# Kernel tuning notes

Hardware: AMD Instinct MI355X
Metric: run time of the kernel (lower is better)

The kernel has to match this reference:

```python
import jax, jax.numpy as jnp
from jax import lax
import numpy as np

DN = ('NCHW', 'OIHW', 'NCHW')

def _bn(x, g, b):
    # BatchNorm2d in training mode: batch statistics, biased variance, eps=1e-5
    m = jnp.mean(x, axis=(0, 2, 3), keepdims=True)
    v = jnp.var(x, axis=(0, 2, 3), keepdims=True)
    return g[None, :, None, None] * (x - m) * lax.rsqrt(v + 1e-5) + b[None, :, None, None]

def _conv(x, w, b, s, p):
    y = lax.conv_general_dilated(x, w, (s, s), [(p, p), (p, p)], dimension_numbers=DN)
    return y + b[None, :, None, None]

def _convt(x, w, b, s, p):
    # torch ConvTranspose2d weight layout [in, out, k, k]; equivalent to
    # input-dilated conv with flipped, transposed kernel and padding k-1-p.
    k = w.shape[2]
    pp = k - 1 - p
    w2 = jnp.flip(w, (2, 3)).transpose(1, 0, 2, 3)  # [out, in, k, k]
    y = lax.conv_general_dilated(x, w2, (1, 1), [(pp, pp), (pp, pp)],
                                 lhs_dilation=(s, s), dimension_numbers=DN)
    return y + b[None, :, None, None]

def setup_inputs() -> dict:
    key = jax.random.key(0)
    ks = jax.random.split(key, 16)
    f32 = jnp.float32
    def rn(i, shape, s):
        return jax.random.normal(ks[i], shape, f32) * s
    K = 256
    inp = {
        'x': jax.random.normal(ks[0], (128, 3, 64, 64), f32),
        'codebook': jax.random.uniform(ks[1], (256, 256), f32, -1.0 / K, 1.0 / K),
        'e_w1': rn(2, (64, 3, 3, 3), 0.19), 'e_b1': jnp.zeros((64,), f32),
        'e_g1': jnp.ones((64,), f32), 'e_be1': jnp.zeros((64,), f32),
        'e_w2': rn(3, (128, 64, 4, 4), 0.031), 'e_b2': jnp.zeros((128,), f32),
        'e_g2': jnp.ones((128,), f32), 'e_be2': jnp.zeros((128,), f32),
        'e_w3': rn(4, (192, 128, 4, 4), 0.022), 'e_b3': jnp.zeros((192,), f32),
        'e_g3': jnp.ones((192,), f32), 'e_be3': jnp.zeros((192,), f32),
        'e_w4': rn(5, (256, 192, 1, 1), 0.072), 'e_b4': jnp.zeros((256,), f32),
        'd_w1': rn(6, (256, 192, 1, 1), 0.062), 'd_b1': jnp.zeros((192,), f32),
        'd_g1': jnp.ones((192,), f32), 'd_be1': jnp.zeros((192,), f32),
        'd_w2': rn(7, (192, 128, 4, 4), 0.018), 'd_b2': jnp.zeros((128,), f32),
        'd_g2': jnp.ones((128,), f32), 'd_be2': jnp.zeros((128,), f32),
        'd_w3': rn(8, (128, 64, 4, 4), 0.022), 'd_b3': jnp.zeros((64,), f32),
        'd_g3': jnp.ones((64,), f32), 'd_be3': jnp.zeros((64,), f32),
        'd_w4': rn(9, (3, 64, 3, 3), 0.042), 'd_b4': jnp.zeros((3,), f32),
    }
    return inp

def reference(x, codebook,
              e_w1, e_b1, e_g1, e_be1, e_w2, e_b2, e_g2, e_be2,
              e_w3, e_b3, e_g3, e_be3, e_w4, e_b4,
              d_w1, d_b1, d_g1, d_be1, d_w2, d_b2, d_g2, d_be2,
              d_w3, d_b3, d_g3, d_be3, d_w4, d_b4):
    # encoder
    h = jax.nn.relu(_bn(_conv(x, e_w1, e_b1, 1, 1), e_g1, e_be1))
    h = jax.nn.relu(_bn(_conv(h, e_w2, e_b2, 2, 1), e_g2, e_be2))
    h = jax.nn.relu(_bn(_conv(h, e_w3, e_b3, 2, 1), e_g3, e_be3))
    h = _conv(h, e_w4, e_b4, 1, 0)  # [B, 256, 16, 16]
    B, C, H, W = h.shape
    Z = h.transpose(0, 2, 3, 1).reshape(-1, C)  # [N, D]
    # fused cdist via ||a||^2 + ||b||^2 - 2ab (argmin invariant to const offsets)
    d2 = (jnp.sum(Z * Z, axis=1, keepdims=True)
          + jnp.sum(codebook * codebook, axis=1)[None, :]
          - 2.0 * (Z @ codebook.T))  # [N, K]
    j = jnp.argmin(d2, axis=1)
    Wj = codebook[j]  # [N, D]
    loss_commit = jnp.mean(jnp.sum((Z - lax.stop_gradient(Wj)) ** 2, axis=1))
    loss_code = jnp.mean(jnp.sum((lax.stop_gradient(Z) - Wj) ** 2, axis=1))
    hq = Wj.reshape(B, H, W, C).transpose(0, 3, 1, 2)
    # decoder
    g = jax.nn.relu(_bn(_convt(hq, d_w1, d_b1, 1, 0), d_g1, d_be1))
    g = jax.nn.relu(_bn(_convt(g, d_w2, d_b2, 2, 1), d_g2, d_be2))
    g = jax.nn.relu(_bn(_convt(g, d_w3, d_b3, 2, 1), d_g3, d_be3))
    g = _conv(g, d_w4, d_b4, 1, 1)  # [B, 3, 64, 64]
    return g, loss_commit, loss_code
```

## Files before the change

### kernel.cpp

```cpp
#include <hip/hip_runtime.h>

#define TPB 256

typedef __attribute__((ext_vector_type(4))) float v4f;
typedef __attribute__((ext_vector_type(8))) short v8s;

__device__ __forceinline__ float us2f(unsigned int u) {
    union { unsigned int i; float f; } w; w.i = u << 16; return w.f;
}
__device__ __forceinline__ unsigned short f2us(float f) {
    union { float ff; unsigned int i; } w; w.ff = f;
    unsigned int u = w.i;
    return (unsigned short)((u + 0x7fffu + ((u >> 16) & 1u)) >> 16);
}
__device__ __forceinline__ void gl_lds16(const unsigned short* g, unsigned short* l) {
    __builtin_amdgcn_global_load_lds(
        (const __attribute__((address_space(1))) unsigned int*)g,
        (__attribute__((address_space(3))) unsigned int*)l, 16, 0, 0);
}

template<int CIN, int COUT, int KK>
__global__ __launch_bounds__(TPB) void repack_w(
    const float* __restrict__ w, unsigned short* __restrict__ o)
{
    int idx = blockIdx.x * TPB + threadIdx.x;
    if (idx >= KK * COUT * CIN) return;
    int ci = idx % CIN;
    int co = (idx / CIN) % COUT;
    int kk = idx / (CIN * COUT);
    o[idx] = f2us(w[((size_t)co * CIN + ci) * KK + kk]);
}
template<int CIN, int COUT>
__global__ __launch_bounds__(TPB) void repack_wt1(
    const float* __restrict__ w, unsigned short* __restrict__ o)
{
    int idx = blockIdx.x * TPB + threadIdx.x;
    if (idx >= CIN * COUT) return;
    int ci = idx % CIN;
    int co = idx / CIN;
    o[idx] = f2us(w[(size_t)ci * COUT + co]);
}
template<int CIN, int COUT, int NCB>
__global__ __launch_bounds__(TPB) void repack_wct2(
    const float* __restrict__ w, unsigned short* __restrict__ o)
{
    constexpr int NCI = CIN / 64;
    int idx = blockIdx.x * TPB + threadIdx.x;
    if (idx >= 16 * COUT * CIN) return;
    int e = idx & 7;
    int lane = (idx >> 3) & 63;
    int seg8 = (idx >> 9) & 7;
    int u = idx >> 12;
    int cb = u % NCB;
    int u2 = u / NCB;
    int cc = u2 % NCI;
    int tk = u2 / NCI;
    int kidx = tk & 3, cls = tk >> 2;
    int lr = lane & 15, lc = lane >> 4;
    int kc = seg8 >> 2, sg = seg8 & 3;
    int co = cb * 64 + sg * 16 + lr;
    int ci = cc * 64 + kc * 32 + lc * 8 + e;
    int ohp = cls >> 1, owp = cls & 1;
    int kh = ((ohp + 1) & 1) + 2 * (kidx >> 1);
    int kw = ((owp + 1) & 1) + 2 * (kidx & 1);
    o[idx] = f2us(w[((size_t)ci * COUT + co) * 16 + kh * 4 + kw]);
}

__global__ __launch_bounds__(TPB) void conv_e1(
    const float* __restrict__ x, const float* __restrict__ w,
    const float* __restrict__ bias, unsigned short* __restrict__ y, int N)
{
    __shared__ float wl[27][64];
    int t = threadIdx.x;
    for (int i = t; i < 27 * 64; i += TPB) {
        int co = i & 63;
        int tap = i >> 6;
        int ci = tap / 9, kk = tap % 9;
        wl[tap][co] = w[((size_t)co * 3 + ci) * 9 + kk];
    }
    __syncthreads();
    int p = blockIdx.x * TPB + t;
    int n = p >> 12, oh = (p >> 6) & 63, ow = p & 63;
    float acc[64];
#pragma unroll
    for (int co = 0; co < 64; co++) acc[co] = bias[co];
    for (int ci = 0; ci < 3; ci++) {
#pragma unroll
        for (int kh = 0; kh < 3; kh++) {
            int ih = oh - 1 + kh;
            if ((unsigned)ih >= 64u) continue;
#pragma unroll
            for (int kw = 0; kw < 3; kw++) {
                int iw = ow - 1 + kw;
                if ((unsigned)iw >= 64u) continue;
                float xv = x[(((size_t)n * 3 + ci) * 64 + ih) * 64 + iw];
                int tap = ci * 9 + kh * 3 + kw;
#pragma unroll
                for (int co = 0; co < 64; co++) acc[co] += xv * wl[tap][co];
            }
        }
    }
    unsigned int* yp = (unsigned int*)(y + (size_t)p * 64);
#pragma unroll
    for (int co = 0; co < 64; co += 2)
        yp[co >> 1] = (unsigned int)f2us(acc[co]) | ((unsigned int)f2us(acc[co + 1]) << 16);
}

template<int CIN, int COUT, int HIN, int WIN, int K, int S, int P, int BN,
         int OUTM, int NYB>
__global__ __launch_bounds__(TPB) void conv_mfma(
    const unsigned short* __restrict__ xin, const unsigned short* __restrict__ wrep,
    const float* __restrict__ bias, void* __restrict__ yout, void* __restrict__ yout2,
    float* __restrict__ part, const unsigned short* __restrict__ zpage, int N)
{
    constexpr int HOUT = (HIN + 2 * P - K) / S + 1;
    constexpr int WOUT = (WIN + 2 * P - K) / S + 1;
    constexpr int RN = BN / 32;
    constexpr int BSEG = BN / 16;
    constexpr int NCI = CIN / 64;
    constexpr int NIT = K * K * NCI;
    __shared__ __align__(16) unsigned short Ab[2][16 * 512];
    __shared__ __align__(16) unsigned short Bb[2][2 * BSEG * 512];

    const int t = threadIdx.x, lane = t & 63, wave = t >> 6;
    const int wm = wave >> 1, wn = wave & 1;
    int m0, co0;
    if (NYB == 2) {
        int g = (int)blockIdx.x >> 3, xs = (int)blockIdx.x & 7;
        co0 = (g & 1) * BN;
        m0 = (((g >> 1) << 3) + xs) * 128;
    } else {
        m0 = (int)blockIdx.x * 128;
        co0 = 0;
    }
    const int lr = lane & 15, lc = lane >> 4;

    int n_[2], oh_[2], ow_[2];
#pragma unroll
    for (int i = 0; i < 2; i++) {
        int r = m0 + (wave + 4 * i) * 16 + lr;
        n_[i] = r / (HOUT * WOUT);
        int rem = r % (HOUT * WOUT);
        oh_[i] = rem / WOUT;
        ow_[i] = rem % WOUT;
    }

    v4f acc[4][RN];
#pragma unroll
    for (int i = 0; i < 4; i++)
#pragma unroll
        for (int j = 0; j < RN; j++)
#pragma unroll
            for (int r = 0; r < 4; r++) acc[i][j][r] = 0.f;

    auto do_stage = [&](int it, int pb) {
        const int kk = it / NCI;
        const int ci0 = (it % NCI) * 64;
        const int kh = kk / K, kw = kk % K;
#pragma unroll
        for (int i = 0; i < 2; i++) {
            int ih = oh_[i] * S - P + kh;
            int iw = ow_[i] * S - P + kw;
            bool av = (unsigned)ih < (unsigned)HIN && (unsigned)iw < (unsigned)WIN;
            const unsigned short* b0 = av
                ? xin + (((size_t)n_[i] * HIN + ih) * WIN + iw) * CIN + lc * 8 + ci0
                : zpage;
            gl_lds16(b0, &Ab[pb][(wave + 4 * i) * 512]);
            gl_lds16(av ? b0 + 32 : zpage, &Ab[pb][(8 + wave + 4 * i) * 512]);
        }
        const unsigned short* wt = wrep + (size_t)kk * COUT * CIN;
#pragma unroll
        for (int i = 0; i < 2; i++) {
            int sgb = wave + 4 * i;
            if (sgb < BSEG) {
                const unsigned short* wb =
                    wt + (size_t)(co0 + sgb * 16 + lr) * CIN + ci0 + lc * 8;
                gl_lds16(wb, &Bb[pb][sgb * 512]);
                gl_lds16(wb + 32, &Bb[pb][(BSEG + sgb) * 512]);
            }
        }
    };

    do_stage(0, 0);
    __syncthreads();

    for (int it = 0; it < NIT; ++it) {
        const int pb = it & 1;
        if (it + 1 < NIT) do_stage(it + 1, pb ^ 1);

#pragma unroll
        for (int kc = 0; kc < 2; kc++) {
            v8s a[4], b[RN];
#pragma unroll
            for (int i = 0; i < 4; i++)
                a[i] = *(const v8s*)&Ab[pb][(kc * 8 + wm * 4 + i) * 512 + lane * 8];
#pragma unroll
            for (int j = 0; j < RN; j++)
                b[j] = *(const v8s*)&Bb[pb][(kc * BSEG + wn * RN + j) * 512 + lane * 8];
#pragma unroll
            for (int i = 0; i < 4; i++)
#pragma unroll
                for (int j = 0; j < RN; j++)
                    acc[i][j] = __builtin_amdgcn_mfma_f32_16x16x32_bf16(a[i], b[j], acc[i][j], 0, 0, 0);
        }
        __syncthreads();
    }

    float sloc[RN], qloc[RN];
#pragma unroll
    for (int j = 0; j < RN; j++) { sloc[j] = 0.f; qloc[j] = 0.f; }

#pragma unroll
    for (int i = 0; i < 4; i++) {
        int mr = wm * 64 + i * 16 + (lane >> 4) * 4;
#pragma unroll
        for (int j = 0; j < RN; j++) {
            int col = co0 + wn * (BN / 2) + j * 16 + (lane & 15);
            float bs = bias[col];
#pragma unroll
            for (int r = 0; r < 4; r++) {
                size_t g = (size_t)(m0 + mr + r) * COUT + col;
                float v = acc[i][j][r] + bs;
                if (OUTM == 2) {
                    unsigned short h = f2us(v);
                    ((unsigned short*)yout)[g] = h;
                    ((unsigned short*)yout2)[g] = f2us(v - us2f(h));
                } else {
                    ((unsigned short*)yout)[g] = f2us(v);
                    sloc[j] += v;
                    qloc[j] += v * v;
                }
            }
        }
    }

    if (OUTM == 0) {
        __syncthreads();
        float* red = (float*)Ab;
        for (int i = t; i < 2 * BN; i += TPB) red[i] = 0.f;
        __syncthreads();
#pragma unroll
        for (int j = 0; j < RN; j++) {
            float s = sloc[j], qv = qloc[j];
            s += __shfl_xor(s, 16); s += __shfl_xor(s, 32);
            qv += __shfl_xor(qv, 16); qv += __shfl_xor(qv, 32);
            if ((lane >> 4) == 0) {
                int cl = wn * (BN / 2) + j * 16 + (lane & 15);
                atomicAdd(&red[cl], s);
                atomicAdd(&red[BN + cl], qv);
            }
        }
        __syncthreads();
        int pb = (NYB == 2) ? (m0 >> 7) : (int)blockIdx.x;
        int PB = (NYB == 2) ? ((int)gridDim.x >> 1) : (int)gridDim.x;
        for (int i = t; i < BN; i += TPB) {
            int col = co0 + i;
            part[(size_t)col * PB + pb] = red[i];
            part[(size_t)(COUT + col) * PB + pb] = red[BN + i];
        }
    }
}

template<int CIN, int COUT, int HIN, int WIN, int NCB, int IN_CLS>
__global__ __launch_bounds__(TPB) void convt_c(
    const unsigned short* __restrict__ xin, const unsigned short* __restrict__ wrep,
    const float* __restrict__ bias, unsigned short* __restrict__ yout,
    float* __restrict__ part, const unsigned short* __restrict__ zpage, int N)
{
    constexpr int NCI = CIN / 64;
    constexpr int NIT = 4 * NCI;
    __shared__ __align__(16) unsigned short Ab[2][16 * 1024];
    __shared__ __align__(16) unsigned short Bb[2][8 * 512];

    const int t = threadIdx.x, lane = t & 63, wave = t >> 6;
    int gdec = (int)blockIdx.x >> 3, xs = (int)blockIdx.x & 7;
    int cb = 0;
    if (NCB == 2) { cb = gdec & 1; gdec >>= 1; }
    const int cls = gdec & 3;
    const int tile = ((gdec >> 2) << 3) + xs;
    const int m0 = tile * 256;
    const int co0 = cb * 64;
    const int ohp = cls >> 1, owp = cls & 1;
    const int khb = (ohp + 1) & 1, kwb = (owp + 1) & 1;
    const int dh0 = (ohp + 1 - khb) >> 1, dw0 = (owp + 1 - kwb) >> 1;
    const int lr = lane & 15, lc = lane >> 4;

    const int jr7 = lane >> 3;
    const int sw = ((lane & 7) ^ jr7) * 8;

    int n_[4], i_[4], j0_[4];
#pragma unroll
    for (int q = 0; q < 4; q++) {
        int r0 = m0 + (wave * 4 + q) * 16;
        n_[q] = r0 / (HIN * WIN);
        int rem = r0 % (HIN * WIN);
        i_[q] = rem / WIN;
        j0_[q] = rem % WIN;
    }

    v4f acc[4][4];
#pragma unroll
    for (int i = 0; i < 4; i++)
#pragma unroll
        for (int j = 0; j < 4; j++)
#pragma unroll
            for (int r = 0; r < 4; r++) acc[i][j][r] = 0.f;

    auto stage = [&](int it, int buf) {
        const int tap = it / NCI, cc = it % NCI;
        const int dh = dh0 - (tap >> 1);
        const int dw = dw0 - (tap & 1);
#pragma unroll
        for (int q = 0; q < 4; q++) {
            const int ih = i_[q] + dh;
            const bool ihv = (unsigned)ih < (unsigned)HIN;
#pragma unroll
            for (int h = 0; h < 2; h++) {
                int iw = j0_[q] + h * 8 + jr7 + dw;
                bool av = ihv && (unsigned)iw < (unsigned)WIN;
                size_t ab;
                if (IN_CLS) {
                    int clsi = ((ih & 1) << 1) | (iw & 1);
                    ab = ((((size_t)clsi * N + n_[q]) * (HIN / 2) + (ih >> 1)) * (WIN / 2)
                         + (iw >> 1)) * CIN;
                } else {
                    ab = (((size_t)n_[q] * HIN + ih) * WIN + iw) * CIN;
                }
                const unsigned short* src = av ? xin + ab + cc * 64 + sw : zpage;
                gl_lds16(src, &Ab[buf][(wave * 4 + q) * 1024 + h * 512]);
            }
        }
        const unsigned short* wb = wrep
            + ((size_t)((cls * 4 + tap) * NCI + cc) * NCB + cb) * 4096;
        gl_lds16(wb + wave * 512 + lane * 8, &Bb[buf][wave * 512]);
        gl_lds16(wb + (4 + wave) * 512 + lane * 8, &Bb[buf][(4 + wave) * 512]);
    };

    auto compute = [&](int it, int buf) {
#pragma unroll
        for (int kc = 0; kc < 2; kc++) {
            v8s a[4], b[4];
#pragma unroll
            for (int i = 0; i < 4; i++)
                a[i] = *(const v8s*)&Ab[buf][(wave * 4 + i) * 1024 + lr * 64
                        + ((kc * 32 + lc * 8) ^ ((lr & 7) << 3))];
#pragma unroll
            for (int j = 0; j < 4; j++)
                b[j] = *(const v8s*)&Bb[buf][(kc * 4 + j) * 512 + lane * 8];
#pragma unroll
            for (int i = 0; i < 4; i++)
#pragma unroll
                for (int j = 0; j < 4; j++)
                    acc[i][j] = __builtin_amdgcn_mfma_f32_16x16x32_bf16(a[i], b[j], acc[i][j], 0, 0, 0);
        }
    };

    stage(0, 0);
    __syncthreads();

#pragma unroll
    for (int it = 0; it < NIT; ++it) {
        const int buf = it & 1;
        if (it + 1 < NIT) stage(it + 1, buf ^ 1);
        compute(it, buf);
        __syncthreads();
    }

    float sloc[4], qloc[4];
#pragma unroll
    for (int j = 0; j < 4; j++) { sloc[j] = 0.f; qloc[j] = 0.f; }

    const size_t clsbase = (size_t)cls * N * HIN * WIN;
#pragma unroll
    for (int i = 0; i < 4; i++) {
        int mr = wave * 64 + i * 16 + (lane >> 4) * 4;
#pragma unroll
        for (int j = 0; j < 4; j++) {
            int col = co0 + j * 16 + (lane & 15);
            float bs = bias[col];
#pragma unroll
            for (int r = 0; r < 4; r++) {
                size_t gi = (clsbase + m0 + mr + r) * COUT + col;
                float v = acc[i][j][r] + bs;
                yout[gi] = f2us(v);
                sloc[j] += v;
                qloc[j] += v * v;
            }
        }
    }

    float* red = (float*)Ab;
    for (int i = t; i < 128; i += TPB) red[i] = 0.f;
    __syncthreads();
#pragma unroll
    for (int j = 0; j < 4; j++) {
        float s = sloc[j], qv = qloc[j];
        s += __shfl_xor(s, 16); s += __shfl_xor(s, 32);
        qv += __shfl_xor(qv, 16); qv += __shfl_xor(qv, 32);
        if ((lane >> 4) == 0) {
            int cl = j * 16 + (lane & 15);
            atomicAdd(&red[cl], s);
            atomicAdd(&red[64 + cl], qv);
        }
    }
    __syncthreads();
    const int TILES = (N * HIN * WIN) >> 8;
    const int PB = 4 * TILES;
    const int pb = cls * TILES + tile;
    for (int i = t; i < 64; i += TPB) {
        part[(size_t)(co0 + i) * PB + pb] = red[i];
        part[(size_t)(COUT + co0 + i) * PB + pb] = red[64 + i];
    }
}

template<int C>
__global__ __launch_bounds__(TPB) void bn_stats_p(
    const unsigned short* __restrict__ x, float* __restrict__ part, int M)
{
    constexpr int GPT = C / 8;
    constexpr int RPB = TPB / GPT;
    constexpr int ACT = RPB * GPT;
    __shared__ float sred[2 * C];
    int t = threadIdx.x;
    for (int i = t; i < 2 * C; i += TPB) sred[i] = 0.f;
    __syncthreads();
    if (t < ACT) {
        int g = t % GPT, rs = t / GPT;
        float s[8], sq[8];
#pragma unroll
        for (int k = 0; k < 8; k++) { s[k] = 0.f; sq[k] = 0.f; }
        for (int row = blockIdx.x * RPB + rs; row < M; row += gridDim.x * RPB) {
            int4 v = *(const int4*)(x + (size_t)row * C + g * 8);
            const unsigned int* vu = (const unsigned int*)&v;
#pragma unroll
            for (int k = 0; k < 4; k++) {
                float f0 = us2f(vu[k] & 0xffffu);
                float f1 = us2f(vu[k] >> 16);
                s[2 * k] += f0; sq[2 * k] += f0 * f0;
                s[2 * k + 1] += f1; sq[2 * k + 1] += f1 * f1;
            }
        }
        int c0 = g * 8;
#pragma unroll
        for (int k = 0; k < 8; k++) {
            atomicAdd(&sred[c0 + k], s[k]);
            atomicAdd(&sred[C + c0 + k], sq[k]);
        }
    }
    __syncthreads();
    int B = gridDim.x;
    for (int i = t; i < 2 * C; i += TPB)
        part[(size_t)i * B + blockIdx.x] = sred[i];
}

template<int C>
__global__ __launch_bounds__(64) void bn_reduce2(
    const float* __restrict__ part, float* __restrict__ st, int B)
{
    int i = blockIdx.x;
    int lane = threadIdx.x;
    float s = 0.f;
    for (int b = lane; b < B; b += 64) s += part[(size_t)i * B + b];
#pragma unroll
    for (int off = 1; off < 64; off <<= 1) s += __shfl_xor(s, off);
    if (lane == 0) st[i] = s;
}

template<int C>
__global__ __launch_bounds__(TPB) void bn_apply_v(
    unsigned short* __restrict__ x, const float* __restrict__ st,
    const float* __restrict__ g, const float* __restrict__ be, int M)
{
    __shared__ float sc[C], sh[C];
    int t = threadIdx.x;
    float cnt = (float)M;
    for (int c = t; c < C; c += TPB) {
        float m = st[c] / cnt;
        float v = st[C + c] / cnt - m * m;
        float s = g[c] * rsqrtf(v + 1e-5f);
        sc[c] = s;
        sh[c] = be[c] - m * s;
    }
    __syncthreads();
    constexpr int GPT = C / 8;
    size_t tot = (size_t)M * GPT;
    for (size_t slot = (size_t)blockIdx.x * TPB + t; slot < tot;
         slot += (size_t)gridDim.x * TPB) {
        int c0 = (int)(slot % GPT) * 8;
        int4 v = *(int4*)(x + slot * 8);
        unsigned int* vu = (unsigned int*)&v;
#pragma unroll
        for (int k = 0; k < 4; k++) {
            float f0 = fmaxf(us2f(vu[k] & 0xffffu) * sc[c0 + 2 * k] + sh[c0 + 2 * k], 0.f);
            float f1 = fmaxf(us2f(vu[k] >> 16) * sc[c0 + 2 * k + 1] + sh[c0 + 2 * k + 1], 0.f);
            vu[k] = (unsigned int)f2us(f0) | ((unsigned int)f2us(f1) << 16);
        }
        *(int4*)(x + slot * 8) = v;
    }
}

__global__ __launch_bounds__(TPB) void cb_prep(
    const float* __restrict__ cb, unsigned short* __restrict__ chb,
    unsigned short* __restrict__ clb, float* __restrict__ cn2)
{
    int j = blockIdx.x, d = threadIdx.x;
    float v = cb[j * 256 + d];
    unsigned short h = f2us(v);
    chb[j * 256 + d] = h;
    clb[j * 256 + d] = f2us(v - us2f(h));
    float s = v * v;
#pragma unroll
    for (int off = 1; off < 64; off <<= 1) s += __shfl_xor(s, off);
    __shared__ float p[4];
    if ((d & 63) == 0) p[d >> 6] = s;
    __syncthreads();
    if (d == 0) cn2[j] = p[0] + p[1] + p[2] + p[3];
}

__global__ __launch_bounds__(TPB) void vq_gemm(
    const unsigned short* __restrict__ zh, const unsigned short* __restrict__ zl,
    const unsigned short* __restrict__ chb, const unsigned short* __restrict__ clb,
    const float* __restrict__ cn2, float* __restrict__ valp, int* __restrict__ idxp)
{
    __shared__ __align__(16) unsigned short Ah[2][8 * 512];
    __shared__ __align__(16) unsigned short Al[2][8 * 512];
    __shared__ __align__(16) unsigned short Bh[2][8 * 512];
    __shared__ __align__(16) unsigned short Bl[2][8 * 512];

    const int t = threadIdx.x, lane = t & 63, wave = t >> 6;
    const int wm = wave >> 1, wn = wave & 1;
    const int gdec = (int)blockIdx.x >> 3, xs = (int)blockIdx.x & 7;
    const int cbk = gdec & 1;
    const int m0 = (((gdec >> 1) << 3) + xs) * 128;
    const int co0 = cbk * 128;
    const int lr = lane & 15, lc = lane >> 4;

    size_t a0 = (size_t)(m0 + wave * 16 + lr) * 256 + lc * 8;
    size_t a1 = a0 + 64 * 256;
    size_t b0 = (size_t)(co0 + wave * 16 + lr) * 256 + lc * 8;
    size_t b1 = b0 + 64 * 256;

    v4f acc[4][4];
#pragma unroll
    for (int i = 0; i < 4; i++)
#pragma unroll
        for (int j = 0; j < 4; j++)
#pragma unroll
            for (int r = 0; r < 4; r++) acc[i][j][r] = 0.f;

    auto do_stage = [&](int ci0, int pb) {
        gl_lds16(zh + a0 + ci0, &Ah[pb][wave * 512]);
        gl_lds16(zh + a1 + ci0, &Ah[pb][(wave + 4) * 512]);
        gl_lds16(zl + a0 + ci0, &Al[pb][wave * 512]);
        gl_lds16(zl + a1 + ci0, &Al[pb][(wave + 4) * 512]);
        gl_lds16(chb + b0 + ci0, &Bh[pb][wave * 512]);
        gl_lds16(chb + b1 + ci0, &Bh[pb][(wave + 4) * 512]);
        gl_lds16(clb + b0 + ci0, &Bl[pb][wave * 512]);
        gl_lds16(clb + b1 + ci0, &Bl[pb][(wave + 4) * 512]);
    };

    do_stage(0, 0);
    __syncthreads();

    for (int s = 0; s < 8; ++s) {
        const int pb = s & 1;
        if (s < 7) do_stage((s + 1) * 32, pb ^ 1);

        v8s a_h[4], a_l[4], b_h[4], b_l[4];
#pragma unroll
        for (int i = 0; i < 4; i++) {
            a_h[i] = *(const v8s*)&Ah[pb][(wm * 4 + i) * 512 + lane * 8];
            a_l[i] = *(const v8s*)&Al[pb][(wm * 4 + i) * 512 + lane * 8];
        }
#pragma unroll
        for (int j = 0; j < 4; j++) {
            b_h[j] = *(const v8s*)&Bh[pb][(wn * 4 + j) * 512 + lane * 8];
            b_l[j] = *(const v8s*)&Bl[pb][(wn * 4 + j) * 512 + lane * 8];
        }
#pragma unroll
        for (int i = 0; i < 4; i++)
#pragma unroll
            for (int j = 0; j < 4; j++) {
                acc[i][j] = __builtin_amdgcn_mfma_f32_16x16x32_bf16(a_h[i], b_h[j], acc[i][j], 0, 0, 0);
                acc[i][j] = __builtin_amdgcn_mfma_f32_16x16x32_bf16(a_h[i], b_l[j], acc[i][j], 0, 0, 0);
                acc[i][j] = __builtin_amdgcn_mfma_f32_16x16x32_bf16(a_l[i], b_h[j], acc[i][j], 0, 0, 0);
            }
        __syncthreads();
    }

#pragma unroll
    for (int i = 0; i < 4; i++) {
#pragma unroll
        for (int r = 0; r < 4; r++) {
            float best = 3.4e38f;
            int bi = 0;
#pragma unroll
            for (int j = 0; j < 4; j++) {
                int col = co0 + wn * 64 + j * 16 + (lane & 15);
                float d = cn2[col] - 2.f * acc[i][j][r];
                if (d < best || (d == best && col < bi)) { best = d; bi = col; }
            }
#pragma unroll
            for (int off = 1; off < 16; off <<= 1) {
                float ov = __shfl_xor(best, off);
                int oi = __shfl_xor(bi, off);
                if (ov < best || (ov == best && oi < bi)) { best = ov; bi = oi; }
            }
            if ((lane & 15) == 0) {
                int row = m0 + wm * 64 + i * 16 + (lane >> 4) * 4 + r;
                valp[(size_t)row * 4 + cbk * 2 + wn] = best;
                idxp[(size_t)row * 4 + cbk * 2 + wn] = bi;
            }
        }
    }
}

__global__ __launch_bounds__(TPB) void vq_gather2(
    const unsigned short* __restrict__ zh, const unsigned short* __restrict__ zl,
    const float* __restrict__ cb, const float* __restrict__ valp,
    const int* __restrict__ idxp, unsigned short* __restrict__ hq,
    float* __restrict__ rowloss)
{
    int row = blockIdx.x * 4 + (threadIdx.x >> 6);
    int lane = threadIdx.x & 63;
    float best = valp[(size_t)row * 4];
    int j = idxp[(size_t)row * 4];
#pragma unroll
    for (int c = 1; c < 4; c++) {
        float v = valp[(size_t)row * 4 + c];
        if (v < best) { best = v; j = idxp[(size_t)row * 4 + c]; }
    }
    ushort4 hv = *(const ushort4*)(zh + (size_t)row * 256 + lane * 4);
    ushort4 lv = *(const ushort4*)(zl + (size_t)row * 256 + lane * 4);
    float4 cv = *(const float4*)(cb + (size_t)j * 256 + lane * 4);
    float z0 = us2f(hv.x) + us2f(lv.x);
    float z1 = us2f(hv.y) + us2f(lv.y);
    float z2 = us2f(hv.z) + us2f(lv.z);
    float z3 = us2f(hv.w) + us2f(lv.w);
    float d0 = z0 - cv.x, d1 = z1 - cv.y, d2 = z2 - cv.z, d3 = z3 - cv.w;
    float d = d0 * d0 + d1 * d1 + d2 * d2 + d3 * d3;
#pragma unroll
    for (int off = 1; off < 64; off <<= 1) d += __shfl_xor(d, off);
    if (lane == 0) rowloss[row] = d;
    ushort4 o;
    o.x = f2us(cv.x); o.y = f2us(cv.y); o.z = f2us(cv.z); o.w = f2us(cv.w);
    *(ushort4*)(hq + (size_t)row * 256 + lane * 4) = o;
}

__global__ __launch_bounds__(TPB) void loss_reduce1(
    const float* __restrict__ rowloss, float* __restrict__ part64)
{
    int t = threadIdx.x;
    int base = blockIdx.x * 512 + t;
    float v = rowloss[base] + rowloss[base + 256];
#pragma unroll
    for (int off = 1; off < 64; off <<= 1) v += __shfl_xor(v, off);
    __shared__ float p[4];
    if ((t & 63) == 0) p[t >> 6] = v;
    __syncthreads();
    if (t == 0) part64[blockIdx.x] = p[0] + p[1] + p[2] + p[3];
}

__global__ __launch_bounds__(64) void loss_finalize(
    const float* __restrict__ part64, float* __restrict__ out2)
{
    float v = part64[threadIdx.x];
    for (int off = 32; off > 0; off >>= 1) v += __shfl_down(v, off);
    if (threadIdx.x == 0) {
        float m = v * (1.0f / 32768.0f);
        out2[0] = m;
        out2[1] = m;
    }
}

__global__ __launch_bounds__(TPB) void conv_d4(
    const unsigned short* __restrict__ xb, const float* __restrict__ w,
    const float* __restrict__ bias, float* __restrict__ out, int N)
{
    __shared__ __align__(16) unsigned short xs[8 * 400 * 8];
    __shared__ float wl[1728];
    int4* xsI = (int4*)xs;
    int t = threadIdx.x;
    for (int i = t; i < 1728; i += TPB) {
        int co = i % 3, ci = (i / 3) % 64, tap = i / 192;
        wl[i] = w[((size_t)co * 64 + ci) * 9 + tap];
    }

    const int n = blockIdx.x >> 4;
    const int tile = blockIdx.x & 15;
    const int th = tile >> 2, tw = tile & 3;
    const int ihh0 = 8 * th - 1, iwh0 = 8 * tw - 1;

    for (int s = t; s < 3200; s += TPB) {
        int cls = s / 800;
        int rem = s % 800;
        int ihh_l = rem / 80;
        int i4 = rem % 80;
        int iwh_l = i4 >> 3, c8 = i4 & 7;
        int ihh_g = ihh0 + ihh_l;
        int iwh_g = iwh0 + iwh_l;
        int4 v;
        if ((unsigned)ihh_g < 32u && (unsigned)iwh_g < 32u) {
            size_t row = (((size_t)cls * 128 + n) * 32 + ihh_g) * 32 + iwh_g;
            v = *(const int4*)(xb + row * 64 + c8 * 8);
        } else {
            v.x = v.y = v.z = v.w = 0;
        }
        xsI[c8 * 400 + cls * 100 + ihh_l * 10 + iwh_l] = v;
    }
    __syncthreads();

    int oh = th * 16 + (t >> 4);
    int ow = tw * 16 + (t & 15);
    float a0 = bias[0], a1 = bias[1], a2 = bias[2];
#pragma unroll
    for (int kh = 0; kh < 3; kh++) {
        int ih = oh - 1 + kh;
#pragma unroll
        for (int kw = 0; kw < 3; kw++) {
            int iw = ow - 1 + kw;
            int clsi = ((ih & 1) << 1) | (iw & 1);
            int base = clsi * 100 + ((ih >> 1) - ihh0) * 10 + ((iw >> 1) - iwh0);
            int tap = kh * 3 + kw;
#pragma unroll
            for (int c8 = 0; c8 < 8; c8++) {
                int4 v = xsI[c8 * 400 + base];
                const unsigned int* vu = (const unsigned int*)&v;
#pragma unroll
                for (int k = 0; k < 4; k++) {
                    unsigned int u = vu[k];
                    float f0 = us2f(u & 0xffffu);
                    float f1 = us2f(u >> 16);
                    const float* wp = &wl[(tap * 64 + c8 * 8 + k * 2) * 3];
                    a0 += f0 * wp[0]; a1 += f0 * wp[1]; a2 += f0 * wp[2];
                    a0 += f1 * wp[3]; a1 += f1 * wp[4]; a2 += f1 * wp[5];
                }
            }
        }
    }
    size_t base = (size_t)n * 3 * 4096 + oh * 64 + ow;
    out[base] = a0;
    out[base + 4096] = a1;
    out[base + 8192] = a2;
}


extern "C" void kernel_launch(void* const* d_in, const int* in_sizes, int n_in,
                              void* d_out, int out_size, void* d_ws, size_t ws_size,
                              hipStream_t stream) {
    const float* x    = (const float*)d_in[0];
    const float* cb   = (const float*)d_in[1];
    const float* e_w1 = (const float*)d_in[2];  const float* e_b1 = (const float*)d_in[3];
    const float* e_g1 = (const float*)d_in[4];  const float* e_be1 = (const float*)d_in[5];
    const float* e_w2 = (const float*)d_in[6];  const float* e_b2 = (const float*)d_in[7];
    const float* e_g2 = (const float*)d_in[8];  const float* e_be2 = (const float*)d_in[9];
    const float* e_w3 = (const float*)d_in[10]; const float* e_b3 = (const float*)d_in[11];
    const float* e_g3 = (const float*)d_in[12]; const float* e_be3 = (const float*)d_in[13];
    const float* e_w4 = (const float*)d_in[14]; const float* e_b4 = (const float*)d_in[15];
    const float* d_w1 = (const float*)d_in[16]; const float* d_b1 = (const float*)d_in[17];
    const float* d_g1 = (const float*)d_in[18]; const float* d_be1 = (const float*)d_in[19];
    const float* d_w2 = (const float*)d_in[20]; const float* d_b2 = (const float*)d_in[21];
    const float* d_g2 = (const float*)d_in[22]; const float* d_be2 = (const float*)d_in[23];
    const float* d_w3 = (const float*)d_in[24]; const float* d_b3 = (const float*)d_in[25];
    const float* d_g3 = (const float*)d_in[26]; const float* d_be3 = (const float*)d_in[27];
    const float* d_w4 = (const float*)d_in[28]; const float* d_b4 = (const float*)d_in[29];

    float* ws = (float*)d_ws;
    unsigned short* h1 = (unsigned short*)(ws);
    unsigned short* g3 = h1;
    unsigned short* h2 = (unsigned short*)(ws + 16777216);
    unsigned short* g2 = h2;
    unsigned short* h3 = (unsigned short*)(ws + 25165824);
    unsigned short* g1 = h3;
    unsigned short* zh = (unsigned short*)(ws + 28311552);
    unsigned short* zl = (unsigned short*)(ws + 32505856);
    unsigned short* hq = (unsigned short*)(ws + 36700160);
    float* stats = ws + 40960000;
    float* cn2 = ws + 40995904;
    unsigned short* chb = (unsigned short*)(ws + 40996160);
    unsigned short* clb = (unsigned short*)(ws + 41028928);
    unsigned short* wrep = (unsigned short*)(ws + 41061696);
    unsigned short* we2 = wrep + 0;
    unsigned short* we3 = wrep + 131072;
    unsigned short* we4 = wrep + 524288;
    unsigned short* wd1 = wrep + 573440;
    unsigned short* wd2 = wrep + 622592;
    unsigned short* wd3 = wrep + 1015808;
    float* part = ws + 41635136;
    float* valp = part;
    int* idxp = (int*)(part + 131072);
    float* rowloss = ws + 50023744;
    float* part64 = ws + 50122048;
    unsigned short* zpage = (unsigned short*)(ws + 50122112);
    float* out = (float*)d_out;
    float* losses = out + 1572864;

    const int N = 128;

    hipMemsetAsync(zpage, 0, 256, stream);

    repack_w<64, 128, 16><<<512, TPB, 0, stream>>>(e_w2, we2);
    repack_w<128, 192, 16><<<1536, TPB, 0, stream>>>(e_w3, we3);
    repack_w<192, 256, 1><<<192, TPB, 0, stream>>>(e_w4, we4);
    repack_wt1<256, 192><<<192, TPB, 0, stream>>>(d_w1, wd1);
    repack_wct2<192, 128, 2><<<1536, TPB, 0, stream>>>(d_w2, wd2);
    repack_wct2<128, 64, 1><<<512, TPB, 0, stream>>>(d_w3, wd3);
    cb_prep<<<256, TPB, 0, stream>>>(cb, chb, clb, cn2);

    conv_e1<<<2048, TPB, 0, stream>>>(x, e_w1, e_b1, h1, N);
    bn_stats_p<64><<<512, TPB, 0, stream>>>(h1, part, 524288);
    bn_reduce2<64><<<128, 64, 0, stream>>>(part, stats + 0 * 512, 512);
    bn_apply_v<64><<<4096, TPB, 0, stream>>>(h1, stats + 0 * 512, e_g1, e_be1, 524288);

    conv_mfma<64, 128, 64, 64, 4, 2, 1, 128, 0, 1>
        <<<1024, TPB, 0, stream>>>(h1, we2, e_b2, h2, nullptr, part, zpage, N);
    bn_reduce2<128><<<256, 64, 0, stream>>>(part, stats + 1 * 512, 1024);
    bn_apply_v<128><<<2048, TPB, 0, stream>>>(h2, stats + 1 * 512, e_g2, e_be2, 131072);

    conv_mfma<128, 192, 32, 32, 4, 2, 1, 96, 0, 2>
        <<<512, TPB, 0, stream>>>(h2, we3, e_b3, h3, nullptr, part, zpage, N);
    bn_reduce2<192><<<384, 64, 0, stream>>>(part, stats + 2 * 512, 256);
    bn_apply_v<192><<<1024, TPB, 0, stream>>>(h3, stats + 2 * 512, e_g3, e_be3, 32768);

    conv_mfma<192, 256, 16, 16, 1, 1, 0, 128, 2, 2>
        <<<512, TPB, 0, stream>>>(h3, we4, e_b4, zh, zl, nullptr, zpage, N);

    vq_gemm<<<512, TPB, 0, stream>>>(zh, zl, chb, clb, cn2, valp, idxp);
    vq_gather2<<<8192, TPB, 0, stream>>>(zh, zl, cb, valp, idxp, hq, rowloss);
    loss_reduce1<<<64, TPB, 0, stream>>>(rowloss, part64);
    loss_finalize<<<1, 64, 0, stream>>>(part64, losses);

    conv_mfma<256, 192, 16, 16, 1, 1, 0, 96, 0, 2>
        <<<512, TPB, 0, stream>>>(hq, wd1, d_b1, g1, nullptr, part, zpage, N);
    bn_reduce2<192><<<384, 64, 0, stream>>>(part, stats + 3 * 512, 256);
    bn_apply_v<192><<<1024, TPB, 0, stream>>>(g1, stats + 3 * 512, d_g1, d_be1, 32768);

    convt_c<192, 128, 16, 16, 2, 0>
        <<<1024, TPB, 0, stream>>>(g1, wd2, d_b2, g2, part, zpage, N);
    bn_reduce2<128><<<256, 64, 0, stream>>>(part, stats + 4 * 512, 512);
    bn_apply_v<128><<<2048, TPB, 0, stream>>>(g2, stats + 4 * 512, d_g2, d_be2, 131072);

    convt_c<128, 64, 32, 32, 1, 1>
        <<<2048, TPB, 0, stream>>>(g2, wd3, d_b3, g3, part, zpage, N);
    bn_reduce2<64><<<128, 64, 0, stream>>>(part, stats + 5 * 512, 2048);
    bn_apply_v<64><<<4096, TPB, 0, stream>>>(g3, stats + 5 * 512, d_g3, d_be3, 524288);

    conv_d4<<<2048, TPB, 0, stream>>>(g3, d_w4, d_b4, out, N);
}
```

Before: 680.0 us.

## Run first encoder conv as bf16 MFMA GEMM via im2col with fused BN stats

Replaces the scalar fp32 direct conv for the first encoder layer with an im2col kernel that writes padded 32-wide bf16 patch rows, followed by an MFMA GEMM against repacked bf16 weights. The GEMM epilogue adds bias, writes bf16 output and accumulates per-channel sum and sum-of-squares partials, so the separate BN statistics pass over h1 is dropped. The final conv's LDS tile stride is also padded (400 to 409, 100 to 102), likely to reduce bank conflicts. Costs: an extra write and read of the im2col buffer, and the input is rounded to bf16 before the GEMM.

After: 651.8 us. 4.1% less time.

```diff
diff --git a/kernel.cpp b/kernel.cpp
--- a/kernel.cpp
+++ b/kernel.cpp
@@ -39,6 +39,14 @@
     int ci = idx % CIN;
     int co = idx / CIN;
     o[idx] = f2us(w[(size_t)ci * COUT + co]);
+}
+__global__ __launch_bounds__(TPB) void repack_we1(
+    const float* __restrict__ w, unsigned short* __restrict__ o)
+{
+    int idx = blockIdx.x * TPB + threadIdx.x;
+    if (idx >= 64 * 32) return;
+    int k = idx & 31, co = idx >> 5;
+    o[idx] = (k < 27) ? f2us(w[co * 27 + k]) : (unsigned short)0;
 }
 template<int CIN, int COUT, int NCB>
 __global__ __launch_bounds__(TPB) void repack_wct2(
@@ -66,44 +74,109 @@
     o[idx] = f2us(w[((size_t)ci * COUT + co) * 16 + kh * 4 + kw]);
 }
 
-__global__ __launch_bounds__(TPB) void conv_e1(
-    const float* __restrict__ x, const float* __restrict__ w,
-    const float* __restrict__ bias, unsigned short* __restrict__ y, int N)
-{
-    __shared__ float wl[27][64];
-    int t = threadIdx.x;
-    for (int i = t; i < 27 * 64; i += TPB) {
-        int co = i & 63;
-        int tap = i >> 6;
-        int ci = tap / 9, kk = tap % 9;
-        wl[tap][co] = w[((size_t)co * 3 + ci) * 9 + kk];
-    }
-    __syncthreads();
-    int p = blockIdx.x * TPB + t;
+__global__ __launch_bounds__(TPB) void im2col_e1(
+    const float* __restrict__ x, unsigned short* __restrict__ A, int N)
+{
+    int p = blockIdx.x * TPB + threadIdx.x;
     int n = p >> 12, oh = (p >> 6) & 63, ow = p & 63;
-    float acc[64];
-#pragma unroll
-    for (int co = 0; co < 64; co++) acc[co] = bias[co];
-    for (int ci = 0; ci < 3; ci++) {
-#pragma unroll
-        for (int kh = 0; kh < 3; kh++) {
-            int ih = oh - 1 + kh;
-            if ((unsigned)ih >= 64u) continue;
-#pragma unroll
-            for (int kw = 0; kw < 3; kw++) {
-                int iw = ow - 1 + kw;
-                if ((unsigned)iw >= 64u) continue;
-                float xv = x[(((size_t)n * 3 + ci) * 64 + ih) * 64 + iw];
-                int tap = ci * 9 + kh * 3 + kw;
-#pragma unroll
-                for (int co = 0; co < 64; co++) acc[co] += xv * wl[tap][co];
-            }
-        }
-    }
-    unsigned int* yp = (unsigned int*)(y + (size_t)p * 64);
-#pragma unroll
-    for (int co = 0; co < 64; co += 2)
-        yp[co >> 1] = (unsigned int)f2us(acc[co]) | ((unsigned int)f2us(acc[co + 1]) << 16);
+    unsigned short row[32];
+#pragma unroll
+    for (int k = 0; k < 27; k++) {
+        int ci = k / 9, tap = k % 9, kh = tap / 3, kw = tap % 3;
+        int ih = oh - 1 + kh, iw = ow - 1 + kw;
+        float v = ((unsigned)ih < 64u && (unsigned)iw < 64u)
+            ? x[(((size_t)n * 3 + ci) * 64 + ih) * 64 + iw] : 0.f;
+        row[k] = f2us(v);
+    }
+#pragma unroll
+    for (int k = 27; k < 32; k++) row[k] = 0;
+    int4* dst = (int4*)(A + (size_t)p * 32);
+    const int4* src = (const int4*)row;
+    dst[0] = src[0]; dst[1] = src[1]; dst[2] = src[2]; dst[3] = src[3];
+}
+
+__global__ __launch_bounds__(TPB) void e1_gemm(
+    const unsigned short* __restrict__ A, const unsigned short* __restrict__ wrep,
+    const float* __restrict__ bias, unsigned short* __restrict__ yout,
+    float* __restrict__ part)
+{
+    __shared__ __align__(16) unsigned short Ab[8 * 512];
+    __shared__ __align__(16) unsigned short Bb[4 * 512];
+
+    const int t = threadIdx.x, lane = t & 63, wave = t >> 6;
+    const int wm = wave >> 1, wn = wave & 1;
+    const int m0 = (int)blockIdx.x * 128;
+    const int lr = lane & 15, lc = lane >> 4;
+
+    gl_lds16(A + (size_t)(m0 + wave * 16 + lr) * 32 + lc * 8, &Ab[wave * 512]);
+    gl_lds16(A + (size_t)(m0 + (wave + 4) * 16 + lr) * 32 + lc * 8, &Ab[(wave + 4) * 512]);
+    gl_lds16(wrep + (size_t)(wave * 16 + lr) * 32 + lc * 8, &Bb[wave * 512]);
+    __syncthreads();
+
+    v4f acc[4][2];
+#pragma unroll
+    for (int i = 0; i < 4; i++)
+#pragma unroll
+        for (int j = 0; j < 2; j++)
+#pragma unroll
+            for (int r = 0; r < 4; r++) acc[i][j][r] = 0.f;
+
+    v8s a[4], b[2];
+#pragma unroll
+    for (int i = 0; i < 4; i++)
+        a[i] = *(const v8s*)&Ab[(wm * 4 + i) * 512 + lane * 8];
+#pragma unroll
+    for (int j = 0; j < 2; j++)
+        b[j] = *(const v8s*)&Bb[(wn * 2 + j) * 512 + lane * 8];
+#pragma unroll
+    for (int i = 0; i < 4; i++)
+#pragma unroll
+        for (int j = 0; j < 2; j++)
+            acc[i][j] = __builtin_amdgcn_mfma_f32_16x16x32_bf16(a[i], b[j], acc[i][j], 0, 0, 0);
+
+    float sloc[2], qloc[2];
+#pragma unroll
+    for (int j = 0; j < 2; j++) { sloc[j] = 0.f; qloc[j] = 0.f; }
+
+#pragma unroll
+    for (int i = 0; i < 4; i++) {
+        int mr = wm * 64 + i * 16 + (lane >> 4) * 4;
+#pragma unroll
+        for (int j = 0; j < 2; j++) {
+            int col = wn * 32 + j * 16 + (lane & 15);
+            float bs = bias[col];
+#pragma unroll
+            for (int r = 0; r < 4; r++) {
+                size_t g = (size_t)(m0 + mr + r) * 64 + col;
+                float v = acc[i][j][r] + bs;
+                yout[g] = f2us(v);
+                sloc[j] += v;
+                qloc[j] += v * v;
+            }
+        }
+    }
+
+    __syncthreads();
+    float* red = (float*)Ab;
+    for (int i = t; i < 128; i += TPB) red[i] = 0.f;
+    __syncthreads();
+#pragma unroll
+    for (int j = 0; j < 2; j++) {
+        float s = sloc[j], qv = qloc[j];
+        s += __shfl_xor(s, 16); s += __shfl_xor(s, 32);
+        qv += __shfl_xor(qv, 16); qv += __shfl_xor(qv, 32);
+        if ((lane >> 4) == 0) {
+            int cl = wn * 32 + j * 16 + (lane & 15);
+            atomicAdd(&red[cl], s);
+            atomicAdd(&red[64 + cl], qv);
+        }
+    }
+    __syncthreads();
+    int PB = (int)gridDim.x, pb = (int)blockIdx.x;
+    for (int i = t; i < 64; i += TPB) {
+        part[(size_t)i * PB + pb] = red[i];
+        part[(size_t)(64 + i) * PB + pb] = red[64 + i];
+    }
 }
 
 template<int CIN, int COUT, int HIN, int WIN, int K, int S, int P, int BN,
@@ -414,46 +487,6 @@
 }
 
 template<int C>
-__global__ __launch_bounds__(TPB) void bn_stats_p(
-    const unsigned short* __restrict__ x, float* __restrict__ part, int M)
-{
-    constexpr int GPT = C / 8;
-    constexpr int RPB = TPB / GPT;
-    constexpr int ACT = RPB * GPT;
-    __shared__ float sred[2 * C];
-    int t = threadIdx.x;
-    for (int i = t; i < 2 * C; i += TPB) sred[i] = 0.f;
-    __syncthreads();
-    if (t < ACT) {
-        int g = t % GPT, rs = t / GPT;
-        float s[8], sq[8];
-#pragma unroll
-        for (int k = 0; k < 8; k++) { s[k] = 0.f; sq[k] = 0.f; }
-        for (int row = blockIdx.x * RPB + rs; row < M; row += gridDim.x * RPB) {
-            int4 v = *(const int4*)(x + (size_t)row * C + g * 8);
-            const unsigned int* vu = (const unsigned int*)&v;
-#pragma unroll
-            for (int k = 0; k < 4; k++) {
-                float f0 = us2f(vu[k] & 0xffffu);
-                float f1 = us2f(vu[k] >> 16);
-                s[2 * k] += f0; sq[2 * k] += f0 * f0;
-                s[2 * k + 1] += f1; sq[2 * k + 1] += f1 * f1;
-            }
-        }
-        int c0 = g * 8;
-#pragma unroll
-        for (int k = 0; k < 8; k++) {
-            atomicAdd(&sred[c0 + k], s[k]);
-            atomicAdd(&sred[C + c0 + k], sq[k]);
-        }
-    }
-    __syncthreads();
-    int B = gridDim.x;
-    for (int i = t; i < 2 * C; i += TPB)
-        part[(size_t)i * B + blockIdx.x] = sred[i];
-}
-
-template<int C>
 __global__ __launch_bounds__(64) void bn_reduce2(
     const float* __restrict__ part, float* __restrict__ st, int B)
 {
@@ -677,7 +710,7 @@
     const unsigned short* __restrict__ xb, const float* __restrict__ w,
     const float* __restrict__ bias, float* __restrict__ out, int N)
 {
-    __shared__ __align__(16) unsigned short xs[8 * 400 * 8];
+    __shared__ __align__(16) unsigned short xs[8 * 409 * 8];
     __shared__ float wl[1728];
     int4* xsI = (int4*)xs;
     int t = threadIdx.x;
@@ -706,7 +739,7 @@
         } else {
             v.x = v.y = v.z = v.w = 0;
         }
-        xsI[c8 * 400 + cls * 100 + ihh_l * 10 + iwh_l] = v;
+        xsI[c8 * 409 + cls * 102 + ihh_l * 10 + iwh_l] = v;
     }
     __syncthreads();
 
@@ -720,11 +753,11 @@
         for (int kw = 0; kw < 3; kw++) {
             int iw = ow - 1 + kw;
             int clsi = ((ih & 1) << 1) | (iw & 1);
-            int base = clsi * 100 + ((ih >> 1) - ihh0) * 10 + ((iw >> 1) - iwh0);
+            int base = clsi * 102 + ((ih >> 1) - ihh0) * 10 + ((iw >> 1) - iwh0);
             int tap = kh * 3 + kw;
 #pragma unroll
             for (int c8 = 0; c8 < 8; c8++) {
-                int4 v = xsI[c8 * 400 + base];
+                int4 v = xsI[c8 * 409 + base];
                 const unsigned int* vu = (const unsigned int*)&v;
 #pragma unroll
                 for (int k = 0; k < 4; k++) {
@@ -774,8 +807,10 @@
     unsigned short* g1 = h3;
     unsigned short* zh = (unsigned short*)(ws + 28311552);
     unsigned short* zl = (unsigned short*)(ws + 32505856);
+    unsigned short* aim = zh;
     unsigned short* hq = (unsigned short*)(ws + 36700160);
     float* stats = ws + 40960000;
+    unsigned short* we1 = (unsigned short*)(ws + 40963072);
     float* cn2 = ws + 40995904;
     unsigned short* chb = (unsigned short*)(ws + 40996160);
     unsigned short* clb = (unsigned short*)(ws + 41028928);
@@ -799,6 +834,7 @@
 
     hipMemsetAsync(zpage, 0, 256, stream);
 
+    repack_we1<<<8, TPB, 0, stream>>>(e_w1, we1);
     repack_w<64, 128, 16><<<512, TPB, 0, stream>>>(e_w2, we2);
     repack_w<128, 192, 16><<<1536, TPB, 0, stream>>>(e_w3, we3);
     repack_w<192, 256, 1><<<192, TPB, 0, stream>>>(e_w4, we4);
@@ -807,9 +843,9 @@
     repack_wct2<128, 64, 1><<<512, TPB, 0, stream>>>(d_w3, wd3);
     cb_prep<<<256, TPB, 0, stream>>>(cb, chb, clb, cn2);
 
-    conv_e1<<<2048, TPB, 0, stream>>>(x, e_w1, e_b1, h1, N);
-    bn_stats_p<64><<<512, TPB, 0, stream>>>(h1, part, 524288);
-    bn_reduce2<64><<<128, 64, 0, stream>>>(part, stats + 0 * 512, 512);
+    im2col_e1<<<2048, TPB, 0, stream>>>(x, aim, N);
+    e1_gemm<<<4096, TPB, 0, stream>>>(aim, we1, e_b1, h1, part);
+    bn_reduce2<64><<<128, 64, 0, stream>>>(part, stats + 0 * 512, 4096);
     bn_apply_v<64><<<4096, TPB, 0, stream>>>(h1, stats + 0 * 512, e_g1, e_be1, 524288);
 
     conv_mfma<64, 128, 64, 64, 4, 2, 1, 128, 0, 1>
```
